# Performance work log

Hardware: AMD Instinct MI355X
Metric: run time of the kernel (lower is better)

## Reference

```python
import jax, jax.numpy as jnp
import numpy as np
from math import sqrt

N_PATCHES = 128
ATTENTION_WINDOW = 10
NEG_FILL = -10000.0


def _mask(L):
    # pid[i] = patch index of position i; channels = L // n_patches
    channels = L // N_PATCHES
    pid = jnp.repeat(jnp.arange(N_PATCHES), channels)
    diff = pid[None, :] - pid[:, None]  # diff[i, j] = pid[j] - pid[i]
    return (diff <= 0) | (diff >= ATTENTION_WINDOW)  # True = masked


def setup_inputs() -> dict:
    key = jax.random.key(0)
    k1, k2, k3 = jax.random.split(key, 3)
    B, H, L, D = 4, 8, 2048, 64
    return {
        "queries": jax.random.normal(k1, (B, H, L, D), dtype=jnp.float32),
        "keys": jax.random.normal(k2, (B, H, L, D), dtype=jnp.float32),
        "values": jax.random.normal(k3, (B, H, L, D), dtype=jnp.float32),
        "log_scale": jnp.asarray(np.log(2.0), dtype=jnp.float32),
    }


def reference(queries, keys, values, log_scale):
    B, H, L, D = queries.shape
    scores = jnp.einsum("bhqd,bhkd->bhqk", queries, keys)
    scale = jnp.clip(jnp.exp(log_scale), 1.0, 30.0) / sqrt(D)
    cmask = _mask(L)[None, None]  # [1,1,L,L]
    pos = jnp.where(cmask, NEG_FILL, scores)
    neg = jnp.where(cmask, NEG_FILL, -scores)
    A = jax.nn.softmax(scale * pos, axis=-1) - jax.nn.softmax(scale * neg, axis=-1)
    return jnp.einsum("bhqk,bhkd->bhqd", A, values)
```

## Files before the change

kernel.cpp:

```cpp
#include <hip/hip_runtime.h>
#include <hip/hip_bf16.h>


#define LSEQ   2048
#define DIM    64
#define CH     16
#define NPATCH 128
#define WIN    9
#define GRP    4
#define KBMAX  192
#define VCOLS  208

#define SK 72
#define SV 216
#define SA 168

typedef __attribute__((ext_vector_type(8))) short bf16x8;
typedef __attribute__((ext_vector_type(4))) float f32x4;

__device__ __forceinline__ unsigned short f2bf1(float a) {
  unsigned int u = __float_as_uint(a);
  u = (u + 0x7fffu + ((u >> 16) & 1u)) >> 16;
  return (unsigned short)u;
}

__device__ __forceinline__ unsigned int pack2bf(float a, float b) {
  unsigned int ua = __float_as_uint(a);
  unsigned int ub = __float_as_uint(b);
  ua = (ua + 0x7fffu + ((ua >> 16) & 1u)) >> 16;
  ub = (ub + 0x7fffu + ((ub >> 16) & 1u)) & 0xffff0000u;
  return ua | ub;
}

__device__ __forceinline__ bf16x8 pack8(float4 a, float4 b) {
  bf16x8 r;
  r[0] = (short)f2bf1(a.x); r[1] = (short)f2bf1(a.y);
  r[2] = (short)f2bf1(a.z); r[3] = (short)f2bf1(a.w);
  r[4] = (short)f2bf1(b.x); r[5] = (short)f2bf1(b.y);
  r[6] = (short)f2bf1(b.z); r[7] = (short)f2bf1(b.w);
  return r;
}

__global__ __launch_bounds__(256, 2)
void signed_attn_kernel(const float* __restrict__ Q,
                        const float* __restrict__ K,
                        const float* __restrict__ V,
                        const float* __restrict__ LS,
                        float* __restrict__ O) {
  __shared__ __align__(16) unsigned short Ks[KBMAX * SK];
  __shared__ __align__(16) unsigned short Vt[DIM * SV];
  __shared__ __align__(16) unsigned short As[GRP * 16 * SA];

  const int g  = blockIdx.x & 31;
  const int bh = blockIdx.x >> 5;
  const int t  = threadIdx.x;
  const int p0 = g * GRP;

  const int kbp = (127 - p0) < 12 ? (127 - p0) : 12;
  const int kb  = kbp * CH;

  const float4* Kg = (const float4*)(K + ((size_t)bh * LSEQ + (size_t)(p0 + 1) * CH) * DIM);
  const float4* Vg = (const float4*)(V + ((size_t)bh * LSEQ + (size_t)(p0 + 1) * CH) * DIM);

  for (int e = t; e < kb * 16; e += 256) {
    int row = e >> 4, d4 = e & 15;
    float4 v = Kg[e];
    *(uint2*)&Ks[row * SK + d4 * 4] =
        make_uint2(pack2bf(v.x, v.y), pack2bf(v.z, v.w));
  }
  {
    const int nq = kb >> 2;
    for (int e = t; e < nq * 16; e += 256) {
      int cq = e >> 4, d4 = e & 15;
      int c = cq << 2;
      float4 v0 = Vg[(c + 0) * 16 + d4];
      float4 v1 = Vg[(c + 1) * 16 + d4];
      float4 v2 = Vg[(c + 2) * 16 + d4];
      float4 v3 = Vg[(c + 3) * 16 + d4];
      int db = d4 << 2;
      *(uint2*)&Vt[(db + 0) * SV + c] = make_uint2(pack2bf(v0.x, v1.x), pack2bf(v2.x, v3.x));
      *(uint2*)&Vt[(db + 1) * SV + c] = make_uint2(pack2bf(v0.y, v1.y), pack2bf(v2.y, v3.y));
      *(uint2*)&Vt[(db + 2) * SV + c] = make_uint2(pack2bf(v0.z, v1.z), pack2bf(v2.z, v3.z));
      *(uint2*)&Vt[(db + 3) * SV + c] = make_uint2(pack2bf(v0.w, v1.w), pack2bf(v2.w, v3.w));
    }
  }
  for (int c = kb + (t >> 6); c < VCOLS; c += 4) Vt[(t & 63) * SV + c] = 0;

  __syncthreads();

  const int w  = t >> 6;
  const int l  = t & 63;
  const int lr = l & 15;
  const int q4 = l >> 4;

  const int p   = p0 + w;
  const int npk = (127 - p) < WIN ? (127 - p) : WIN;
  float* Og = O + ((size_t)bh * LSEQ + (size_t)p * CH) * DIM;

  if (npk == 0) {
#pragma unroll
    for (int n = 0; n < 4; n++)
#pragma unroll
      for (int r = 0; r < 4; r++)
        Og[(q4 * 4 + r) * DIM + n * 16 + lr] = 0.f;
    return;
  }

  const float scale = fminf(30.f, fmaxf(1.f, __expf(LS[0]))) * 0.125f;
  const int koff = w * CH;

  const float* Qg = Q + ((size_t)bh * LSEQ + (size_t)p * CH) * DIM;
  bf16x8 qa[2];
#pragma unroll
  for (int s = 0; s < 2; s++) {
    const float* qp = Qg + lr * DIM + q4 * 8 + 32 * s;
    qa[s] = pack8(*(const float4*)qp, *(const float4*)(qp + 4));
  }

  f32x4 sacc[WIN];
#pragma unroll
  for (int tl = 0; tl < WIN; tl++) {
    f32x4 acc = {0.f, 0.f, 0.f, 0.f};
#pragma unroll
    for (int s = 0; s < 2; s++) {
      bf16x8 b = *(const bf16x8*)&Ks[(koff + tl * 16 + lr) * SK + q4 * 8 + 32 * s];
      acc = __builtin_amdgcn_mfma_f32_16x16x32_bf16(qa[s], b, acc, 0, 0, 0);
    }
    sacc[tl] = acc;
  }

  float mx[4], mi[4];
#pragma unroll
  for (int r = 0; r < 4; r++) { mx[r] = -1e30f; mi[r] = 1e30f; }
#pragma unroll
  for (int tl = 0; tl < WIN; tl++) {
    bool val = tl < npk;
#pragma unroll
    for (int r = 0; r < 4; r++) {
      float s = sacc[tl][r];
      mx[r] = fmaxf(mx[r], val ? s : -1e30f);
      mi[r] = fminf(mi[r], val ? s : 1e30f);
    }
  }
#pragma unroll
  for (int off = 1; off < 16; off <<= 1)
#pragma unroll
    for (int r = 0; r < 4; r++) {
      mx[r] = fmaxf(mx[r], __shfl_xor(mx[r], off));
      mi[r] = fminf(mi[r], __shfl_xor(mi[r], off));
    }

  float mp[4], mn[4], sp[4], sn[4];
#pragma unroll
  for (int r = 0; r < 4; r++) {
    mp[r] = scale * mx[r];
    mn[r] = -scale * mi[r];
    sp[r] = 0.f; sn[r] = 0.f;
  }

  f32x4 e2a[WIN];
#pragma unroll
  for (int tl = 0; tl < WIN; tl++) {
    bool val = tl < npk;
#pragma unroll
    for (int r = 0; r < 4; r++) {
      float s  = sacc[tl][r];
      float e1 = __expf(scale * s - mp[r]);
      float e2 = __expf(-scale * s - mn[r]);
      e1 = val ? e1 : 0.f;
      e2 = val ? e2 : 0.f;
      sacc[tl][r] = e1;
      e2a[tl][r]  = e2;
      sp[r] += e1; sn[r] += e2;
    }
  }
#pragma unroll
  for (int off = 1; off < 16; off <<= 1)
#pragma unroll
    for (int r = 0; r < 4; r++) {
      sp[r] += __shfl_xor(sp[r], off);
      sn[r] += __shfl_xor(sn[r], off);
    }

  float rp[4], rn[4];
#pragma unroll
  for (int r = 0; r < 4; r++) { rp[r] = 1.0f / sp[r]; rn[r] = 1.0f / sn[r]; }

  unsigned short* Aw = As + w * 16 * SA;
#pragma unroll
  for (int tl = 0; tl < WIN; tl++)
#pragma unroll
    for (int r = 0; r < 4; r++) {
      float a = sacc[tl][r] * rp[r] - e2a[tl][r] * rn[r];
      Aw[(q4 * 4 + r) * SA + tl * 16 + lr] = f2bf1(a);
    }
#pragma unroll
  for (int r = 0; r < 4; r++)
    Aw[(q4 * 4 + r) * SA + 144 + lr] = 0;

  f32x4 oacc[4] = {{0,0,0,0},{0,0,0,0},{0,0,0,0},{0,0,0,0}};
#pragma unroll
  for (int s = 0; s < 5; s++) {
    bf16x8 a = *(const bf16x8*)&Aw[lr * SA + s * 32 + q4 * 8];
#pragma unroll
    for (int n = 0; n < 4; n++) {
      bf16x8 b = *(const bf16x8*)&Vt[(n * 16 + lr) * SV + koff + s * 32 + q4 * 8];
      oacc[n] = __builtin_amdgcn_mfma_f32_16x16x32_bf16(a, b, oacc[n], 0, 0, 0);
    }
  }
#pragma unroll
  for (int n = 0; n < 4; n++)
#pragma unroll
    for (int r = 0; r < 4; r++)
      Og[(q4 * 4 + r) * DIM + n * 16 + lr] = oacc[n][r];
}

extern "C" void kernel_launch(void* const* d_in, const int* in_sizes, int n_in,
                              void* d_out, int out_size, void* d_ws, size_t ws_size,
                              hipStream_t stream) {
  const float* Q  = (const float*)d_in[0];
  const float* K  = (const float*)d_in[1];
  const float* V  = (const float*)d_in[2];
  const float* LS = (const float*)d_in[3];
  float* O = (float*)d_out;
  signed_attn_kernel<<<dim3(1024), dim3(256), 0, stream>>>(Q, K, V, LS, O);
}
```

Measured before the change: 110.2 us.

## Load K fragments directly from global, enlarge patch group, recompute exponentials

```diff
diff --git a/kernel.cpp b/kernel.cpp
--- a/kernel.cpp
+++ b/kernel.cpp
@@ -5,14 +5,11 @@
 #define LSEQ   2048
 #define DIM    64
 #define CH     16
-#define NPATCH 128
 #define WIN    9
-#define GRP    4
-#define KBMAX  192
-#define VCOLS  208
-
-#define SK 72
-#define SV 216
+#define GRP    8
+#define VCOLS  272
+
+#define SV 280
 #define SA 168
 
 typedef __attribute__((ext_vector_type(8))) short bf16x8;
@@ -41,36 +38,28 @@
   return r;
 }
 
-__global__ __launch_bounds__(256, 2)
+__global__ __launch_bounds__(512, 4)
 void signed_attn_kernel(const float* __restrict__ Q,
                         const float* __restrict__ K,
                         const float* __restrict__ V,
                         const float* __restrict__ LS,
                         float* __restrict__ O) {
-  __shared__ __align__(16) unsigned short Ks[KBMAX * SK];
   __shared__ __align__(16) unsigned short Vt[DIM * SV];
   __shared__ __align__(16) unsigned short As[GRP * 16 * SA];
 
-  const int g  = blockIdx.x & 31;
-  const int bh = blockIdx.x >> 5;
+  const int g  = blockIdx.x & 15;
+  const int bh = blockIdx.x >> 4;
   const int t  = threadIdx.x;
   const int p0 = g * GRP;
 
-  const int kbp = (127 - p0) < 12 ? (127 - p0) : 12;
+  const int kbp = (127 - p0) < 17 ? (127 - p0) : 17;
   const int kb  = kbp * CH;
 
-  const float4* Kg = (const float4*)(K + ((size_t)bh * LSEQ + (size_t)(p0 + 1) * CH) * DIM);
   const float4* Vg = (const float4*)(V + ((size_t)bh * LSEQ + (size_t)(p0 + 1) * CH) * DIM);
 
-  for (int e = t; e < kb * 16; e += 256) {
-    int row = e >> 4, d4 = e & 15;
-    float4 v = Kg[e];
-    *(uint2*)&Ks[row * SK + d4 * 4] =
-        make_uint2(pack2bf(v.x, v.y), pack2bf(v.z, v.w));
-  }
   {
     const int nq = kb >> 2;
-    for (int e = t; e < nq * 16; e += 256) {
+    for (int e = t; e < nq * 16; e += 512) {
       int cq = e >> 4, d4 = e & 15;
       int c = cq << 2;
       float4 v0 = Vg[(c + 0) * 16 + d4];
@@ -84,9 +73,7 @@
       *(uint2*)&Vt[(db + 3) * SV + c] = make_uint2(pack2bf(v0.w, v1.w), pack2bf(v2.w, v3.w));
     }
   }
-  for (int c = kb + (t >> 6); c < VCOLS; c += 4) Vt[(t & 63) * SV + c] = 0;
-
-  __syncthreads();
+  for (int c = kb + (t >> 6); c < VCOLS; c += 8) Vt[(t & 63) * SV + c] = 0;
 
   const int w  = t >> 6;
   const int l  = t & 63;
@@ -95,6 +82,17 @@
 
   const int p   = p0 + w;
   const int npk = (127 - p) < WIN ? (127 - p) : WIN;
+
+  const float* Qg = Q + ((size_t)bh * LSEQ + (size_t)p * CH) * DIM;
+  bf16x8 qa[2];
+#pragma unroll
+  for (int s = 0; s < 2; s++) {
+    const float* qp = Qg + lr * DIM + q4 * 8 + 32 * s;
+    qa[s] = pack8(*(const float4*)qp, *(const float4*)(qp + 4));
+  }
+
+  __syncthreads();
+
   float* Og = O + ((size_t)bh * LSEQ + (size_t)p * CH) * DIM;
 
   if (npk == 0) {
@@ -109,21 +107,16 @@
   const float scale = fminf(30.f, fmaxf(1.f, __expf(LS[0]))) * 0.125f;
   const int koff = w * CH;
 
-  const float* Qg = Q + ((size_t)bh * LSEQ + (size_t)p * CH) * DIM;
-  bf16x8 qa[2];
-#pragma unroll
-  for (int s = 0; s < 2; s++) {
-    const float* qp = Qg + lr * DIM + q4 * 8 + 32 * s;
-    qa[s] = pack8(*(const float4*)qp, *(const float4*)(qp + 4));
-  }
-
+  const float* Kb = K + ((size_t)bh * LSEQ + (size_t)(p + 1) * CH) * DIM;
   f32x4 sacc[WIN];
 #pragma unroll
   for (int tl = 0; tl < WIN; tl++) {
+    int row = (tl < npk ? tl * 16 : 0) + lr;
+    const float* kp = Kb + row * DIM + q4 * 8;
     f32x4 acc = {0.f, 0.f, 0.f, 0.f};
 #pragma unroll
     for (int s = 0; s < 2; s++) {
-      bf16x8 b = *(const bf16x8*)&Ks[(koff + tl * 16 + lr) * SK + q4 * 8 + 32 * s];
+      bf16x8 b = pack8(*(const float4*)(kp + 32 * s), *(const float4*)(kp + 32 * s + 4));
       acc = __builtin_amdgcn_mfma_f32_16x16x32_bf16(qa[s], b, acc, 0, 0, 0);
     }
     sacc[tl] = acc;
@@ -158,7 +151,6 @@
     sp[r] = 0.f; sn[r] = 0.f;
   }
 
-  f32x4 e2a[WIN];
 #pragma unroll
   for (int tl = 0; tl < WIN; tl++) {
     bool val = tl < npk;
@@ -167,11 +159,8 @@
       float s  = sacc[tl][r];
       float e1 = __expf(scale * s - mp[r]);
       float e2 = __expf(-scale * s - mn[r]);
-      e1 = val ? e1 : 0.f;
-      e2 = val ? e2 : 0.f;
-      sacc[tl][r] = e1;
-      e2a[tl][r]  = e2;
-      sp[r] += e1; sn[r] += e2;
+      sp[r] += val ? e1 : 0.f;
+      sn[r] += val ? e2 : 0.f;
     }
   }
 #pragma unroll
@@ -188,12 +177,17 @@
 
   unsigned short* Aw = As + w * 16 * SA;
 #pragma unroll
-  for (int tl = 0; tl < WIN; tl++)
-#pragma unroll
-    for (int r = 0; r < 4; r++) {
-      float a = sacc[tl][r] * rp[r] - e2a[tl][r] * rn[r];
+  for (int tl = 0; tl < WIN; tl++) {
+    bool val = tl < npk;
+#pragma unroll
+    for (int r = 0; r < 4; r++) {
+      float s  = sacc[tl][r];
+      float e1 = __expf(scale * s - mp[r]);
+      float e2 = __expf(-scale * s - mn[r]);
+      float a  = val ? (e1 * rp[r] - e2 * rn[r]) : 0.f;
       Aw[(q4 * 4 + r) * SA + tl * 16 + lr] = f2bf1(a);
     }
+  }
 #pragma unroll
   for (int r = 0; r < 4; r++)
     Aw[(q4 * 4 + r) * SA + 144 + lr] = 0;
@@ -223,5 +217,5 @@
   const float* V  = (const float*)d_in[2];
   const float* LS = (const float*)d_in[3];
   float* O = (float*)d_out;
-  signed_attn_kernel<<<dim3(1024), dim3(256), 0, stream>>>(Q, K, V, LS, O);
-}
+  signed_attn_kernel<<<dim3(512), dim3(512), 0, stream>>>(Q, K, V, LS, O);
+}
```

Measured after the change: 110.3 us. About the same (+0.1%).
